# Optimization experiments

Measured on AMD Instinct MI355X. Metric: run time of the kernel, lower is better.

Reference implementation:

```python
import jax, jax.numpy as jnp
import numpy as np

EMBEDDING_DIM = 768
ATTENTION_HEADS = 12
N = 1024
BATCH = 8
D_HEAD = EMBEDDING_DIM // ATTENTION_HEADS  # 64


def setup_inputs() -> dict:
    key = jax.random.key(0)
    ks = jax.random.split(key, 6)
    return {
        "embeddings": jax.random.normal(ks[0], (BATCH, N, EMBEDDING_DIM), dtype=jnp.float32),
        "B_matrix": jax.random.normal(ks[1], (1, ATTENTION_HEADS, N, N), dtype=jnp.float32),
        "WQ": jax.random.normal(ks[2], (EMBEDDING_DIM, EMBEDDING_DIM), dtype=jnp.float32),
        "WK": jax.random.normal(ks[3], (EMBEDDING_DIM, EMBEDDING_DIM), dtype=jnp.float32),
        "WV": jax.random.normal(ks[4], (EMBEDDING_DIM, EMBEDDING_DIM), dtype=jnp.float32),
        "WO": jax.random.normal(ks[5], (EMBEDDING_DIM, EMBEDDING_DIM), dtype=jnp.float32),
    }


def reference(embeddings, B_matrix, WQ, WK, WV, WO):
    H, d = ATTENTION_HEADS, D_HEAD
    scale = 1.0 / jnp.sqrt(jnp.float32(d))
    # Faithful to original: reshape(-1, H, N, d) directly (NOT a head-split transpose).
    Qh = (embeddings @ WQ).reshape(-1, H, N, d)   # [B, H, N, d]
    Kh = (embeddings @ WK).reshape(-1, H, N, d)
    Vh = (embeddings @ WV).reshape(-1, H, N, d)
    scores = jnp.einsum("bhnd,bhmd->bhnm", Qh, Kh) * scale  # [B, H, N, N]
    attn = jax.nn.softmax(scores + B_matrix, axis=-1)
    Hc = jnp.einsum("bhnm,bhmd->bhnd", attn, Vh)  # [B, H, N, d]
    Hc = Hc.transpose(0, 2, 1, 3).reshape(-1, N, EMBEDDING_DIM)  # [B, N, E]
    return Hc @ WO
```

## Files before the change

### kernel.cpp

```cpp
#include <hip/hip_runtime.h>
#include <math.h>

#define EDIM 768
#define NSEQ 1024
#define NB 8
#define NH 12
#define DH 64

typedef __attribute__((ext_vector_type(8))) short bh8;
typedef __attribute__((ext_vector_type(4))) float f4;
typedef __attribute__((ext_vector_type(8))) unsigned short us8;
typedef __attribute__((ext_vector_type(4))) unsigned short us4;

#define MFMA(a, b, c) __builtin_amdgcn_mfma_f32_16x16x32_bf16((bh8)(a), (bh8)(b), (c), 0, 0, 0)

__device__ __forceinline__ unsigned short f2bf(float x) {
    union { float f; unsigned u; } v; v.f = x;
    unsigned r = v.u + 0x7fff + ((v.u >> 16) & 1);
    return (unsigned short)(r >> 16);
}
__device__ __forceinline__ float bf2f(unsigned short b) {
    union { float f; unsigned u; } v; v.u = ((unsigned)b) << 16;
    return v.f;
}

__global__ __launch_bounds__(256)
void conv_emb(const float* __restrict__ E, unsigned short* __restrict__ Eh,
              unsigned short* __restrict__ El)
{
    size_t idx = ((size_t)blockIdx.x * 256 + threadIdx.x) * 4;
    float4 v = *(const float4*)&E[idx];
    us4 h, l;
    h.x = f2bf(v.x); l.x = f2bf(v.x - bf2f(h.x));
    h.y = f2bf(v.y); l.y = f2bf(v.y - bf2f(h.y));
    h.z = f2bf(v.z); l.z = f2bf(v.z - bf2f(h.z));
    h.w = f2bf(v.w); l.w = f2bf(v.w - bf2f(h.w));
    *(us4*)&Eh[idx] = h;
    *(us4*)&El[idx] = l;
}

__global__ __launch_bounds__(256)
void conv_w(const float* __restrict__ W0, const float* __restrict__ W1,
            const float* __restrict__ W2, const float* __restrict__ W3,
            unsigned short* __restrict__ Wbase)
{
    const int z = blockIdx.z;
    const float* __restrict__ W = (z == 0) ? W0 : (z == 1) ? W1 : (z == 2) ? W2 : W3;
    unsigned short* __restrict__ Wh = Wbase + (size_t)z * 2 * (EDIM * EDIM);
    unsigned short* __restrict__ Wl = Wh + (EDIM * EDIM);

    __shared__ float T[64][65];
    const int t = threadIdx.x;
    const int n0 = blockIdx.x * 64, k0 = blockIdx.y * 64;

#pragma unroll
    for (int rr = 0; rr < 4; rr++) {
        int row = rr * 16 + (t >> 4);
        int c4  = (t & 15) * 4;
        float4 v = *(const float4*)&W[(size_t)(k0 + row) * EDIM + n0 + c4];
        T[row][c4 + 0] = v.x; T[row][c4 + 1] = v.y;
        T[row][c4 + 2] = v.z; T[row][c4 + 3] = v.w;
    }
    __syncthreads();
#pragma unroll
    for (int rr = 0; rr < 4; rr++) {
        int nn = rr * 16 + (t >> 4);
        int k4 = (t & 15) * 4;
        us4 h, l;
        float v0 = T[k4 + 0][nn], v1 = T[k4 + 1][nn],
              v2 = T[k4 + 2][nn], v3 = T[k4 + 3][nn];
        h.x = f2bf(v0); l.x = f2bf(v0 - bf2f(h.x));
        h.y = f2bf(v1); l.y = f2bf(v1 - bf2f(h.y));
        h.z = f2bf(v2); l.z = f2bf(v2 - bf2f(h.z));
        h.w = f2bf(v3); l.w = f2bf(v3 - bf2f(h.w));
        size_t o = (size_t)(n0 + nn) * EDIM + k0 + k4;
        *(us4*)&Wh[o] = h;
        *(us4*)&Wl[o] = l;
    }
}

__global__ __launch_bounds__(256)
void qkv_gemm(const unsigned short* __restrict__ Eh, const unsigned short* __restrict__ El,
              const unsigned short* __restrict__ Wbase,
              unsigned short* __restrict__ Qh, unsigned short* __restrict__ Ql,
              unsigned short* __restrict__ Kh, unsigned short* __restrict__ Kl,
              unsigned short* __restrict__ Vt)
{
    const int bid = blockIdx.x;
    const int xcd = bid & 7, j = bid >> 3;
    const int mblk = xcd * 8 + (j / 18);
    const int rest = j % 18;
    const int nblk = rest % 6, z = rest / 6;

    const unsigned short* __restrict__ Wh = Wbase + (size_t)z * 2 * (EDIM * EDIM);
    const unsigned short* __restrict__ Wl = Wh + (EDIM * EDIM);

    __shared__ unsigned short Ahq[4][128][8], Alq[4][128][8];
    __shared__ unsigned short Bhq[4][128][8], Blq[4][128][8];

    const int t = threadIdx.x;
    const int wave = t >> 6, lane = t & 63;
    const int quad = lane >> 4, l16 = lane & 15;
    const int wm = (wave >> 1) * 64, wn = (wave & 1) * 64;
    const int m0 = mblk * 128, n0 = nblk * 128;

    const int sr = t >> 1, q0 = (t & 1) * 2;

    f4 acc[4][4];
#pragma unroll
    for (int i = 0; i < 4; i++)
#pragma unroll
        for (int j2 = 0; j2 < 4; j2++) acc[i][j2] = (f4){0.f, 0.f, 0.f, 0.f};

    for (int k0 = 0; k0 < EDIM; k0 += 32) {
        const size_t ao = (size_t)(m0 + sr) * EDIM + k0 + q0 * 8;
        const size_t bo = (size_t)(n0 + sr) * EDIM + k0 + q0 * 8;
        us8 a0 = *(const us8*)&Eh[ao], a1 = *(const us8*)&Eh[ao + 8];
        us8 b0 = *(const us8*)&Wh[bo], b1 = *(const us8*)&Wh[bo + 8];
        us8 a2, a3, b2, b3;
        if (z != 2) {
            a2 = *(const us8*)&El[ao]; a3 = *(const us8*)&El[ao + 8];
            b2 = *(const us8*)&Wl[bo]; b3 = *(const us8*)&Wl[bo + 8];
        }
        __syncthreads();
        *(us8*)&Ahq[q0][sr][0] = a0; *(us8*)&Ahq[q0 + 1][sr][0] = a1;
        *(us8*)&Bhq[q0][sr][0] = b0; *(us8*)&Bhq[q0 + 1][sr][0] = b1;
        if (z != 2) {
            *(us8*)&Alq[q0][sr][0] = a2; *(us8*)&Alq[q0 + 1][sr][0] = a3;
            *(us8*)&Blq[q0][sr][0] = b2; *(us8*)&Blq[q0 + 1][sr][0] = b3;
        }
        __syncthreads();

        bh8 aH[4], bH[4];
#pragma unroll
        for (int mt = 0; mt < 4; mt++)
            aH[mt] = *(const bh8*)&Ahq[quad][wm + mt * 16 + l16][0];
#pragma unroll
        for (int nt = 0; nt < 4; nt++)
            bH[nt] = *(const bh8*)&Bhq[quad][wn + nt * 16 + l16][0];

        if (z != 2) {
            bh8 aL[4], bL[4];
#pragma unroll
            for (int mt = 0; mt < 4; mt++)
                aL[mt] = *(const bh8*)&Alq[quad][wm + mt * 16 + l16][0];
#pragma unroll
            for (int nt = 0; nt < 4; nt++)
                bL[nt] = *(const bh8*)&Blq[quad][wn + nt * 16 + l16][0];
#pragma unroll
            for (int mt = 0; mt < 4; mt++)
#pragma unroll
                for (int nt = 0; nt < 4; nt++) {
                    acc[mt][nt] = MFMA(aH[mt], bH[nt], acc[mt][nt]);
                    acc[mt][nt] = MFMA(aH[mt], bL[nt], acc[mt][nt]);
                    acc[mt][nt] = MFMA(aL[mt], bH[nt], acc[mt][nt]);
                }
        } else {
#pragma unroll
            for (int mt = 0; mt < 4; mt++)
#pragma unroll
                for (int nt = 0; nt < 4; nt++)
                    acc[mt][nt] = MFMA(aH[mt], bH[nt], acc[mt][nt]);
        }
    }

#pragma unroll
    for (int mt = 0; mt < 4; mt++)
#pragma unroll
        for (int nt = 0; nt < 4; nt++)
#pragma unroll
            for (int r = 0; r < 4; r++) {
                int row = m0 + wm + mt * 16 + quad * 4 + r;
                int col = n0 + wn + nt * 16 + l16;
                float v = acc[mt][nt][r];
                if (z == 2) {
                    int bb = row >> 10, nr = row & 1023;
                    int g = nr * 12 + (col >> 6);
                    int hh = g >> 10, key = g & 1023, dim = col & 63;
                    Vt[(((size_t)(bb * NH + hh)) * DH + dim) * NSEQ + key] = f2bf(v);
                } else {
                    unsigned short h = f2bf(v);
                    unsigned short l = f2bf(v - bf2f(h));
                    size_t o = (size_t)row * EDIM + col;
                    if (z == 0) { Qh[o] = h; Ql[o] = l; }
                    else        { Kh[o] = h; Kl[o] = l; }
                }
            }
}

__global__ __launch_bounds__(256)
void attn_mfma(const unsigned short* __restrict__ Qh, const unsigned short* __restrict__ Ql,
               const unsigned short* __restrict__ Kh, const unsigned short* __restrict__ Kl,
               const unsigned short* __restrict__ Vt, const float* __restrict__ Bm,
               unsigned short* __restrict__ Hc)
{
    const int bid = blockIdx.x;
    const int xcd = bid & 7, j = bid >> 3;
    const int combo = xcd * 12 + (j >> 4);
    const int rt = j & 15;
    const int h = combo >> 3, b = combo & 7;
    const int r0 = rt * 64;

    __shared__ unsigned short Khs[64][72], Kls[64][72];
    __shared__ unsigned short Vts[64][72];
    __shared__ unsigned short Ps[4][16][68];

    const int t = threadIdx.x;
    const int wave = t >> 6, lane = t & 63;
    const int quad = lane >> 4, l16 = lane & 15;
    const int wr = wave * 16;

    const int srow = t >> 2, sseg = (t & 3) * 16;

    const size_t hb = (size_t)b * (NSEQ * EDIM) + (size_t)h * (NSEQ * DH);
    const size_t vb = (((size_t)(b * NH + h)) * DH) * NSEQ;

    bh8 qfh[2], qfl[2];
    {
        const size_t qo = hb + (size_t)(r0 + srow) * DH + sseg;
        us8 q0 = *(const us8*)&Qh[qo], q1 = *(const us8*)&Qh[qo + 8];
        us8 q2 = *(const us8*)&Ql[qo], q3 = *(const us8*)&Ql[qo + 8];
        *(us8*)&Khs[srow][sseg] = q0; *(us8*)&Khs[srow][sseg + 8] = q1;
        *(us8*)&Kls[srow][sseg] = q2; *(us8*)&Kls[srow][sseg + 8] = q3;
        __syncthreads();
#pragma unroll
        for (int ks = 0; ks < 2; ks++) {
            qfh[ks] = *(const bh8*)&Khs[wr + l16][ks * 32 + quad * 8];
            qfl[ks] = *(const bh8*)&Kls[wr + l16][ks * 32 + quad * 8];
        }
    }

    float m[4] = {-3e38f, -3e38f, -3e38f, -3e38f};
    float lsum[4] = {0.f, 0.f, 0.f, 0.f};
    f4 o[4];
#pragma unroll
    for (int dt = 0; dt < 4; dt++) o[dt] = (f4){0.f, 0.f, 0.f, 0.f};

    const float* bb = Bm + ((size_t)h << 20) + ((size_t)(r0 + wr + quad * 4) << 10) + l16;

    for (int kt = 0; kt < 16; kt++) {
        const int c0 = kt * 64;
        const size_t ko = hb + (size_t)(c0 + srow) * DH + sseg;
        const size_t vo = vb + (size_t)srow * NSEQ + c0 + sseg;
        us8 k0v = *(const us8*)&Kh[ko], k1v = *(const us8*)&Kh[ko + 8];
        us8 k2v = *(const us8*)&Kl[ko], k3v = *(const us8*)&Kl[ko + 8];
        us8 v0v = *(const us8*)&Vt[vo], v1v = *(const us8*)&Vt[vo + 8];
        __syncthreads();
        *(us8*)&Khs[srow][sseg] = k0v; *(us8*)&Khs[srow][sseg + 8] = k1v;
        *(us8*)&Kls[srow][sseg] = k2v; *(us8*)&Kls[srow][sseg + 8] = k3v;
        *(us8*)&Vts[srow][sseg] = v0v; *(us8*)&Vts[srow][sseg + 8] = v1v;
        __syncthreads();

        f4 s[4];
#pragma unroll
        for (int ct = 0; ct < 4; ct++) {
            bh8 kh0 = *(const bh8*)&Khs[ct * 16 + l16][quad * 8];
            bh8 kh1 = *(const bh8*)&Khs[ct * 16 + l16][32 + quad * 8];
            bh8 kl0 = *(const bh8*)&Kls[ct * 16 + l16][quad * 8];
            bh8 kl1 = *(const bh8*)&Kls[ct * 16 + l16][32 + quad * 8];
            f4 a = (f4){0.f, 0.f, 0.f, 0.f};
            a = MFMA(qfh[0], kh0, a); a = MFMA(qfh[1], kh1, a);
            a = MFMA(qfl[0], kh0, a); a = MFMA(qfl[1], kh1, a);
            a = MFMA(qfh[0], kl0, a); a = MFMA(qfh[1], kl1, a);
            s[ct] = a;
        }
#pragma unroll
        for (int ct = 0; ct < 4; ct++)
#pragma unroll
            for (int r = 0; r < 4; r++)
                s[ct][r] = fmaf(s[ct][r], 0.125f, bb[(size_t)r * NSEQ + c0 + ct * 16]);

        float alpha[4];
#pragma unroll
        for (int r = 0; r < 4; r++) {
            float mx = fmaxf(fmaxf(s[0][r], s[1][r]), fmaxf(s[2][r], s[3][r]));
            mx = fmaxf(mx, __shfl_xor(mx, 1));
            mx = fmaxf(mx, __shfl_xor(mx, 2));
            mx = fmaxf(mx, __shfl_xor(mx, 4));
            mx = fmaxf(mx, __shfl_xor(mx, 8));
            float mn = fmaxf(m[r], mx);
            alpha[r] = __expf(m[r] - mn);
            m[r] = mn;
        }
#pragma unroll
        for (int ct = 0; ct < 4; ct++)
#pragma unroll
            for (int r = 0; r < 4; r++)
                s[ct][r] = __expf(s[ct][r] - m[r]);
#pragma unroll
        for (int r = 0; r < 4; r++) {
            float ls = s[0][r] + s[1][r] + s[2][r] + s[3][r];
            ls += __shfl_xor(ls, 1);
            ls += __shfl_xor(ls, 2);
            ls += __shfl_xor(ls, 4);
            ls += __shfl_xor(ls, 8);
            lsum[r] = lsum[r] * alpha[r] + ls;
        }
#pragma unroll
        for (int dt = 0; dt < 4; dt++)
#pragma unroll
            for (int r = 0; r < 4; r++) o[dt][r] *= alpha[r];

#pragma unroll
        for (int ct = 0; ct < 4; ct++)
#pragma unroll
            for (int r = 0; r < 4; r++)
                Ps[wave][quad * 4 + r][ct * 16 + l16] = f2bf(s[ct][r]);

        bh8 p0 = *(const bh8*)&Ps[wave][l16][quad * 8];
        bh8 p1 = *(const bh8*)&Ps[wave][l16][32 + quad * 8];
#pragma unroll
        for (int dt = 0; dt < 4; dt++) {
            bh8 v0 = *(const bh8*)&Vts[dt * 16 + l16][quad * 8];
            bh8 v1 = *(const bh8*)&Vts[dt * 16 + l16][32 + quad * 8];
            o[dt] = MFMA(p0, v0, o[dt]);
            o[dt] = MFMA(p1, v1, o[dt]);
        }
    }

#pragma unroll
    for (int r = 0; r < 4; r++) lsum[r] = 1.f / lsum[r];
#pragma unroll
    for (int dt = 0; dt < 4; dt++)
#pragma unroll
        for (int r = 0; r < 4; r++) {
            int row = r0 + wr + quad * 4 + r;
            int col = h * DH + dt * 16 + l16;
            Hc[(size_t)(b * NSEQ + row) * EDIM + col] = f2bf(o[dt][r] * lsum[r]);
        }
}

__global__ __launch_bounds__(256)
void out_gemm(const unsigned short* __restrict__ A, const unsigned short* __restrict__ Wh,
              float* __restrict__ C)
{
    const int bid = blockIdx.x;
    const int xcd = bid & 7, j = bid >> 3;
    const int mblk = xcd * 8 + (j / 6);
    const int nblk = j % 6;

    __shared__ unsigned short Ahq[4][128][8];
    __shared__ unsigned short Bhq[4][128][8];

    const int t = threadIdx.x;
    const int wave = t >> 6, lane = t & 63;
    const int quad = lane >> 4, l16 = lane & 15;
    const int wm = (wave >> 1) * 64, wn = (wave & 1) * 64;
    const int m0 = mblk * 128, n0 = nblk * 128;
    const int sr = t >> 1, q0 = (t & 1) * 2;

    f4 acc[4][4];
#pragma unroll
    for (int i = 0; i < 4; i++)
#pragma unroll
        for (int j2 = 0; j2 < 4; j2++) acc[i][j2] = (f4){0.f, 0.f, 0.f, 0.f};

    for (int k0 = 0; k0 < EDIM; k0 += 32) {
        const size_t ao = (size_t)(m0 + sr) * EDIM + k0 + q0 * 8;
        const size_t bo = (size_t)(n0 + sr) * EDIM + k0 + q0 * 8;
        us8 a0 = *(const us8*)&A[ao], a1 = *(const us8*)&A[ao + 8];
        us8 b0 = *(const us8*)&Wh[bo], b1 = *(const us8*)&Wh[bo + 8];
        __syncthreads();
        *(us8*)&Ahq[q0][sr][0] = a0; *(us8*)&Ahq[q0 + 1][sr][0] = a1;
        *(us8*)&Bhq[q0][sr][0] = b0; *(us8*)&Bhq[q0 + 1][sr][0] = b1;
        __syncthreads();

        bh8 aF[4], bF[4];
#pragma unroll
        for (int mt = 0; mt < 4; mt++)
            aF[mt] = *(const bh8*)&Ahq[quad][wm + mt * 16 + l16][0];
#pragma unroll
        for (int nt = 0; nt < 4; nt++)
            bF[nt] = *(const bh8*)&Bhq[quad][wn + nt * 16 + l16][0];
#pragma unroll
        for (int mt = 0; mt < 4; mt++)
#pragma unroll
            for (int nt = 0; nt < 4; nt++)
                acc[mt][nt] = MFMA(aF[mt], bF[nt], acc[mt][nt]);
    }

#pragma unroll
    for (int mt = 0; mt < 4; mt++)
#pragma unroll
        for (int nt = 0; nt < 4; nt++)
#pragma unroll
            for (int r = 0; r < 4; r++) {
                int row = m0 + wm + mt * 16 + quad * 4 + r;
                int col = n0 + wn + nt * 16 + l16;
                C[(size_t)row * EDIM + col] = acc[mt][nt][r];
            }
}

extern "C" void kernel_launch(void* const* d_in, const int* in_sizes, int n_in,
                              void* d_out, int out_size, void* d_ws, size_t ws_size,
                              hipStream_t stream)
{
    const float* emb = (const float*)d_in[0];
    const float* Bm  = (const float*)d_in[1];
    const float* WQ  = (const float*)d_in[2];
    const float* WK  = (const float*)d_in[3];
    const float* WV  = (const float*)d_in[4];
    const float* WO  = (const float*)d_in[5];
    float* out = (float*)d_out;

    const size_t SZ = (size_t)NB * NSEQ * EDIM;
    const size_t WSZ = (size_t)EDIM * EDIM;

    unsigned short* p  = (unsigned short*)d_ws;
    unsigned short* Eh = p;                  p += SZ;
    unsigned short* El = p;                  p += SZ;
    unsigned short* Wb = p;                  p += 8 * WSZ;
    unsigned short* Qh = p;                  p += SZ;
    unsigned short* Ql = p;                  p += SZ;
    unsigned short* Kh = p;                  p += SZ;
    unsigned short* Kl = p;                  p += SZ;
    unsigned short* Vt = p;                  p += SZ;
    unsigned short* Hc = Eh;

    conv_emb<<<dim3(SZ / (256 * 4)), dim3(256), 0, stream>>>(emb, Eh, El);
    conv_w<<<dim3(EDIM / 64, EDIM / 64, 4), dim3(256), 0, stream>>>(WQ, WK, WV, WO, Wb);

    qkv_gemm<<<dim3(1152), dim3(256), 0, stream>>>(
        Eh, El, Wb, Qh, Ql, Kh, Kl, Vt);

    attn_mfma<<<dim3(1536), dim3(256), 0, stream>>>(
        Qh, Ql, Kh, Kl, Vt, Bm, Hc);

    out_gemm<<<dim3(384), dim3(256), 0, stream>>>(
        Hc, Wb + 6 * WSZ, out);
}
```

Baseline: 412.2 us.

## Prefetch next tile into registers and use DPP row reductions in softmax

Applies register-level software pipelining to the projection GEMM, the attention loop and the output GEMM. The next K-slice (or K/V tile) is issued from global memory right after the shared-memory store, so its latency overlaps the MFMA work on the current tile. The attention kernel also loads the bias values up front and replaces shfl_xor max/sum reductions with DPP row_shr moves. This costs more live registers, which may lower occupancy, and the last iteration does a wasted wrap-around load.

```diff
diff --git a/kernel.cpp b/kernel.cpp
--- a/kernel.cpp
+++ b/kernel.cpp
@@ -22,6 +22,27 @@
 __device__ __forceinline__ float bf2f(unsigned short b) {
     union { float f; unsigned u; } v; v.u = ((unsigned)b) << 16;
     return v.f;
+}
+
+template <int C>
+__device__ __forceinline__ float dppmov(float x) {
+    union { int i; float f; } u; u.f = x;
+    u.i = __builtin_amdgcn_update_dpp(0, u.i, C, 0xF, 0xF, true);
+    return u.f;
+}
+__device__ __forceinline__ float rowmax16(float x) {
+    x = fmaxf(x, dppmov<0x121>(x));
+    x = fmaxf(x, dppmov<0x122>(x));
+    x = fmaxf(x, dppmov<0x124>(x));
+    x = fmaxf(x, dppmov<0x128>(x));
+    return x;
+}
+__device__ __forceinline__ float rowsum16(float x) {
+    x += dppmov<0x121>(x);
+    x += dppmov<0x122>(x);
+    x += dppmov<0x124>(x);
+    x += dppmov<0x128>(x);
+    return x;
 }
 
 __global__ __launch_bounds__(256)
@@ -112,16 +133,18 @@
 #pragma unroll
         for (int j2 = 0; j2 < 4; j2++) acc[i][j2] = (f4){0.f, 0.f, 0.f, 0.f};
 
-    for (int k0 = 0; k0 < EDIM; k0 += 32) {
-        const size_t ao = (size_t)(m0 + sr) * EDIM + k0 + q0 * 8;
-        const size_t bo = (size_t)(n0 + sr) * EDIM + k0 + q0 * 8;
-        us8 a0 = *(const us8*)&Eh[ao], a1 = *(const us8*)&Eh[ao + 8];
-        us8 b0 = *(const us8*)&Wh[bo], b1 = *(const us8*)&Wh[bo + 8];
-        us8 a2, a3, b2, b3;
-        if (z != 2) {
-            a2 = *(const us8*)&El[ao]; a3 = *(const us8*)&El[ao + 8];
-            b2 = *(const us8*)&Wl[bo]; b3 = *(const us8*)&Wl[bo + 8];
-        }
+    const size_t abase = (size_t)(m0 + sr) * EDIM + q0 * 8;
+    const size_t bbase = (size_t)(n0 + sr) * EDIM + q0 * 8;
+
+    us8 a0 = *(const us8*)&Eh[abase], a1 = *(const us8*)&Eh[abase + 8];
+    us8 b0 = *(const us8*)&Wh[bbase], b1 = *(const us8*)&Wh[bbase + 8];
+    us8 a2, a3, b2, b3;
+    if (z != 2) {
+        a2 = *(const us8*)&El[abase]; a3 = *(const us8*)&El[abase + 8];
+        b2 = *(const us8*)&Wl[bbase]; b3 = *(const us8*)&Wl[bbase + 8];
+    }
+
+    for (int it = 0; it < 24; it++) {
         __syncthreads();
         *(us8*)&Ahq[q0][sr][0] = a0; *(us8*)&Ahq[q0 + 1][sr][0] = a1;
         *(us8*)&Bhq[q0][sr][0] = b0; *(us8*)&Bhq[q0 + 1][sr][0] = b1;
@@ -130,6 +153,16 @@
             *(us8*)&Blq[q0][sr][0] = b2; *(us8*)&Blq[q0 + 1][sr][0] = b3;
         }
         __syncthreads();
+
+        {
+            const int kn = (it < 23) ? (it + 1) * 32 : 0;
+            a0 = *(const us8*)&Eh[abase + kn]; a1 = *(const us8*)&Eh[abase + kn + 8];
+            b0 = *(const us8*)&Wh[bbase + kn]; b1 = *(const us8*)&Wh[bbase + kn + 8];
+            if (z != 2) {
+                a2 = *(const us8*)&El[abase + kn]; a3 = *(const us8*)&El[abase + kn + 8];
+                b2 = *(const us8*)&Wl[bbase + kn]; b3 = *(const us8*)&Wl[bbase + kn + 8];
+            }
+        }
 
         bh8 aH[4], bH[4];
 #pragma unroll
@@ -215,6 +248,9 @@
     const size_t hb = (size_t)b * (NSEQ * EDIM) + (size_t)h * (NSEQ * DH);
     const size_t vb = (((size_t)(b * NH + h)) * DH) * NSEQ;
 
+    const size_t kbase = hb + (size_t)srow * DH + sseg;
+    const size_t vbase = vb + (size_t)srow * NSEQ + sseg;
+
     bh8 qfh[2], qfl[2];
     {
         const size_t qo = hb + (size_t)(r0 + srow) * DH + sseg;
@@ -230,6 +266,10 @@
         }
     }
 
+    us8 k0v = *(const us8*)&Kh[kbase],     k1v = *(const us8*)&Kh[kbase + 8];
+    us8 k2v = *(const us8*)&Kl[kbase],     k3v = *(const us8*)&Kl[kbase + 8];
+    us8 v0v = *(const us8*)&Vt[vbase],     v1v = *(const us8*)&Vt[vbase + 8];
+
     float m[4] = {-3e38f, -3e38f, -3e38f, -3e38f};
     float lsum[4] = {0.f, 0.f, 0.f, 0.f};
     f4 o[4];
@@ -240,16 +280,28 @@
 
     for (int kt = 0; kt < 16; kt++) {
         const int c0 = kt * 64;
-        const size_t ko = hb + (size_t)(c0 + srow) * DH + sseg;
-        const size_t vo = vb + (size_t)srow * NSEQ + c0 + sseg;
-        us8 k0v = *(const us8*)&Kh[ko], k1v = *(const us8*)&Kh[ko + 8];
-        us8 k2v = *(const us8*)&Kl[ko], k3v = *(const us8*)&Kl[ko + 8];
-        us8 v0v = *(const us8*)&Vt[vo], v1v = *(const us8*)&Vt[vo + 8];
         __syncthreads();
         *(us8*)&Khs[srow][sseg] = k0v; *(us8*)&Khs[srow][sseg + 8] = k1v;
         *(us8*)&Kls[srow][sseg] = k2v; *(us8*)&Kls[srow][sseg + 8] = k3v;
         *(us8*)&Vts[srow][sseg] = v0v; *(us8*)&Vts[srow][sseg + 8] = v1v;
         __syncthreads();
+
+        {
+            const int cn = ((kt + 1) & 15) * 64;
+            k0v = *(const us8*)&Kh[kbase + (size_t)cn * DH];
+            k1v = *(const us8*)&Kh[kbase + (size_t)cn * DH + 8];
+            k2v = *(const us8*)&Kl[kbase + (size_t)cn * DH];
+            k3v = *(const us8*)&Kl[kbase + (size_t)cn * DH + 8];
+            v0v = *(const us8*)&Vt[vbase + cn];
+            v1v = *(const us8*)&Vt[vbase + cn + 8];
+        }
+
+        float bv[4][4];
+#pragma unroll
+        for (int ct = 0; ct < 4; ct++)
+#pragma unroll
+            for (int r = 0; r < 4; r++)
+                bv[ct][r] = bb[(size_t)r * NSEQ + c0 + ct * 16];
 
         f4 s[4];
 #pragma unroll
@@ -268,16 +320,13 @@
         for (int ct = 0; ct < 4; ct++)
 #pragma unroll
             for (int r = 0; r < 4; r++)
-                s[ct][r] = fmaf(s[ct][r], 0.125f, bb[(size_t)r * NSEQ + c0 + ct * 16]);
+                s[ct][r] = fmaf(s[ct][r], 0.125f, bv[ct][r]);
 
         float alpha[4];
 #pragma unroll
         for (int r = 0; r < 4; r++) {
             float mx = fmaxf(fmaxf(s[0][r], s[1][r]), fmaxf(s[2][r], s[3][r]));
-            mx = fmaxf(mx, __shfl_xor(mx, 1));
-            mx = fmaxf(mx, __shfl_xor(mx, 2));
-            mx = fmaxf(mx, __shfl_xor(mx, 4));
-            mx = fmaxf(mx, __shfl_xor(mx, 8));
+            mx = rowmax16(mx);
             float mn = fmaxf(m[r], mx);
             alpha[r] = __expf(m[r] - mn);
             m[r] = mn;
@@ -289,11 +338,7 @@
                 s[ct][r] = __expf(s[ct][r] - m[r]);
 #pragma unroll
         for (int r = 0; r < 4; r++) {
-            float ls = s[0][r] + s[1][r] + s[2][r] + s[3][r];
-            ls += __shfl_xor(ls, 1);
-            ls += __shfl_xor(ls, 2);
-            ls += __shfl_xor(ls, 4);
-            ls += __shfl_xor(ls, 8);
+            float ls = rowsum16(s[0][r] + s[1][r] + s[2][r] + s[3][r]);
             lsum[r] = lsum[r] * alpha[r] + ls;
         }
 #pragma unroll
@@ -355,15 +400,23 @@
 #pragma unroll
         for (int j2 = 0; j2 < 4; j2++) acc[i][j2] = (f4){0.f, 0.f, 0.f, 0.f};
 
-    for (int k0 = 0; k0 < EDIM; k0 += 32) {
-        const size_t ao = (size_t)(m0 + sr) * EDIM + k0 + q0 * 8;
-        const size_t bo = (size_t)(n0 + sr) * EDIM + k0 + q0 * 8;
-        us8 a0 = *(const us8*)&A[ao], a1 = *(const us8*)&A[ao + 8];
-        us8 b0 = *(const us8*)&Wh[bo], b1 = *(const us8*)&Wh[bo + 8];
+    const size_t abase = (size_t)(m0 + sr) * EDIM + q0 * 8;
+    const size_t bbase = (size_t)(n0 + sr) * EDIM + q0 * 8;
+
+    us8 a0 = *(const us8*)&A[abase],  a1 = *(const us8*)&A[abase + 8];
+    us8 b0 = *(const us8*)&Wh[bbase], b1 = *(const us8*)&Wh[bbase + 8];
+
+    for (int it = 0; it < 24; it++) {
         __syncthreads();
         *(us8*)&Ahq[q0][sr][0] = a0; *(us8*)&Ahq[q0 + 1][sr][0] = a1;
         *(us8*)&Bhq[q0][sr][0] = b0; *(us8*)&Bhq[q0 + 1][sr][0] = b1;
         __syncthreads();
+
+        {
+            const int kn = (it < 23) ? (it + 1) * 32 : 0;
+            a0 = *(const us8*)&A[abase + kn];  a1 = *(const us8*)&A[abase + kn + 8];
+            b0 = *(const us8*)&Wh[bbase + kn]; b1 = *(const us8*)&Wh[bbase + kn + 8];
+        }
 
         bh8 aF[4], bF[4];
 #pragma unroll
```

New measurement: 337.4 us. 1.22x faster.
